# Kernel optimization log

Hardware: AMD Instinct MI355X
Metric: run time of the kernel (lower is better)

## Reference

```python
import jax, jax.numpy as jnp
import numpy as np

B, N, D = 2, 1024, 256
H, HD = 8, 32
FF = 1024
DEPTH = 2
RELH = 64  # rel-bias MLP hidden
SCALE = HD ** -0.5
EPS = 1e-5


def _ln(x, g, b):
    m = jnp.mean(x, axis=-1, keepdims=True)
    v = jnp.mean((x - m) ** 2, axis=-1, keepdims=True)
    return (x - m) * jax.lax.rsqrt(v + EPS) * g + b


def _rotary(n):
    half = HD // 2
    inv_freq = 1.0 / (10000.0 ** (jnp.arange(0, HD, 2, dtype=jnp.float32) / HD))  # [half]
    freqs = jnp.arange(n, dtype=jnp.float32)[:, None] * inv_freq[None, :]  # [n, half]
    return jnp.sin(freqs)[None, None], jnp.cos(freqs)[None, None]  # [1,1,n,half]


def _rope(t, sin, cos):
    t1, t2 = t[..., : HD // 2], t[..., HD // 2 :]
    return jnp.concatenate([t1 * cos - t2 * sin, t2 * cos + t1 * sin], axis=-1)


def setup_inputs() -> dict:
    key = jax.random.key(0)
    ks = jax.random.split(key, 20)
    s = 0.02
    inp = {
        "x": jax.random.normal(ks[0], (B, N, D), jnp.float32),
        "coords": jax.random.uniform(ks[1], (B, N, 2), jnp.float32),
        "velocities": jax.random.normal(ks[2], (B, N, 2), jnp.float32),
        "ln1_g": jnp.ones((DEPTH, D), jnp.float32),
        "ln1_b": jnp.zeros((DEPTH, D), jnp.float32),
        "Wqkv": jax.random.normal(ks[3], (DEPTH, D, 3 * H * HD), jnp.float32) * s,
        "relW1": jax.random.normal(ks[4], (DEPTH, 5, RELH), jnp.float32) * s,
        "relb1": jnp.zeros((DEPTH, RELH), jnp.float32),
        "relW2": jax.random.normal(ks[5], (DEPTH, RELH, H), jnp.float32) * s,
        "relb2": jnp.zeros((DEPTH, H), jnp.float32),
        "Wout": jax.random.normal(ks[6], (DEPTH, H * HD, D), jnp.float32) * s,
        "bout": jnp.zeros((DEPTH, D), jnp.float32),
        "ln2_g": jnp.ones((DEPTH, D), jnp.float32),
        "ln2_b": jnp.zeros((DEPTH, D), jnp.float32),
        "Wf1": jax.random.normal(ks[7], (DEPTH, D, FF), jnp.float32) * s,
        "bf1": jnp.zeros((DEPTH, FF), jnp.float32),
        "Wf2": jax.random.normal(ks[8], (DEPTH, FF, D), jnp.float32) * s,
        "bf2": jnp.zeros((DEPTH, D), jnp.float32),
    }
    return inp


def reference(x, coords, velocities, ln1_g, ln1_b, Wqkv, relW1, relb1, relW2,
              relb2, Wout, bout, ln2_g, ln2_b, Wf1, bf1, Wf2, bf2):
    sin, cos = _rotary(N)
    # pairwise relational features, shared across layers: [B,N,N,5]
    dx = coords[:, :, None, :] - coords[:, None, :, :]
    dist = jnp.linalg.norm(dx, axis=-1, keepdims=True)
    dv = velocities[:, :, None, :] - velocities[:, None, :, :]
    feats = jnp.concatenate([dx, dist, dv], axis=-1)
    for l in range(DEPTH):
        h = _ln(x, ln1_g[l], ln1_b[l])
        qkv = h @ Wqkv[l]  # [B,N,3*H*HD]
        q, k, v = jnp.split(qkv, 3, axis=-1)
        q, k, v = [t.reshape(B, N, H, HD).transpose(0, 2, 1, 3) for t in (q, k, v)]
        q = _rope(q, sin, cos)
        k = _rope(k, sin, cos)
        # relational bias MLP: [B,N,N,5] -> [B,N,N,H] -> [B,H,N,N]
        rel = jax.nn.gelu(feats @ relW1[l] + relb1[l], approximate=False) @ relW2[l] + relb2[l]
        rel = rel.transpose(0, 3, 1, 2)
        scores = jnp.einsum("bhid,bhjd->bhij", q, k) * SCALE + rel
        probs = jax.nn.softmax(scores, axis=-1)
        probs = jnp.nan_to_num(probs, nan=0.0)
        out = jnp.einsum("bhij,bhjd->bhid", probs, v)
        out = out.transpose(0, 2, 1, 3).reshape(B, N, H * HD)
        x = out @ Wout[l] + bout[l] + x
        h2 = _ln(x, ln2_g[l], ln2_b[l])
        x = jax.nn.gelu(h2 @ Wf1[l] + bf1[l], approximate=False) @ Wf2[l] + bf2[l] + x
    return x
```

## Files before the change

kernel.cpp:

```cpp
#include <hip/hip_runtime.h>
#include <math.h>

#define BN_ 2
#define NN 1024
#define DDIM 256
#define HH 8
#define HDIM 32
#define FFD 1024
#define EPSV 1e-5f
#define SCALEV 0.17677669529663687f

typedef __attribute__((ext_vector_type(8))) short s16x8;
typedef __attribute__((ext_vector_type(4))) short s16x4;
typedef __attribute__((ext_vector_type(4))) float f32x4;
typedef __attribute__((ext_vector_type(2))) _Float16 h2;
typedef __attribute__((ext_vector_type(8))) _Float16 f16x8;

__device__ __forceinline__ float gelu_f(float x){
  return 0.5f*x*(1.0f+erff(x*0.70710678118654752f));
}
__device__ __forceinline__ unsigned int pack_bf16(float lo, float hi){
  unsigned int ul = __float_as_uint(lo), uh = __float_as_uint(hi);
  ul += 0x7fff + ((ul>>16)&1);
  uh += 0x7fff + ((uh>>16)&1);
  return (ul>>16) | (uh & 0xffff0000u);
}
__device__ __forceinline__ unsigned short f2bf(float x){
  unsigned int u = __float_as_uint(x);
  u += 0x7fff + ((u>>16)&1);
  return (unsigned short)(u>>16);
}
__device__ __forceinline__ float bf2f(unsigned short u){
  return __uint_as_float(((unsigned int)u)<<16);
}
__device__ __forceinline__ unsigned int packtr(float lo, float hi){
  return __builtin_amdgcn_perm(__float_as_uint(hi), __float_as_uint(lo), 0x07060302u);
}
__device__ __forceinline__ f32x4 mfma16(s16x8 a, s16x8 b, f32x4 c){
  return __builtin_amdgcn_mfma_f32_16x16x32_bf16(a,b,c,0,0,0);
}
__device__ __forceinline__ f32x4 mfma16h(f16x8 a, f16x8 b, f32x4 c){
  return __builtin_amdgcn_mfma_f32_16x16x32_f16(a,b,c,0,0,0);
}

__global__ __launch_bounds__(256) void ln_kernel(const float* __restrict__ x,
    const float* __restrict__ g, const float* __restrict__ b,
    unsigned short* __restrict__ out){
  int row = blockIdx.x, tid = threadIdx.x;
  float val = x[(size_t)row*DDIM + tid];
  float s = val;
  #pragma unroll
  for (int o=32;o;o>>=1) s += __shfl_xor(s,o);
  __shared__ float sb[4], sb2[4];
  if ((tid&63)==0) sb[tid>>6]=s;
  __syncthreads();
  float mean = (sb[0]+sb[1]+sb[2]+sb[3]) * (1.0f/DDIM);
  float d = val-mean;
  float vs = d*d;
  #pragma unroll
  for (int o=32;o;o>>=1) vs += __shfl_xor(vs,o);
  if ((tid&63)==0) sb2[tid>>6]=vs;
  __syncthreads();
  float var = (sb2[0]+sb2[1]+sb2[2]+sb2[3]) * (1.0f/DDIM);
  out[(size_t)row*DDIM + tid] = f2bf(d*rsqrtf(var+EPSV)*g[tid]+b[tid]);
}

__global__ __launch_bounds__(256) void rope_table(float* __restrict__ sint, float* __restrict__ cost){
  int idx = blockIdx.x*256+threadIdx.x;
  int i = idx >> 4, d = idx & 15;
  float freq = (float)i * powf(10000.0f, -(float)d/16.0f);
  sint[idx]=sinf(freq); cost[idx]=cosf(freq);
}

__global__ __launch_bounds__(256) void wt_convert(const float* __restrict__ in,
    unsigned short* __restrict__ out, int K, int NC, int scaleCols, float scaleVal){
  __shared__ float tile[32][33];
  int tn0 = blockIdx.x*32;
  int tk0 = blockIdx.y*32;
  size_t loff = (size_t)blockIdx.z * K * NC;
  int t = threadIdx.x;
  int col = t & 31, rr = t >> 5;
  #pragma unroll
  for (int i=0;i<4;++i){
    int row = rr + i*8;
    tile[row][col] = in[loff + (size_t)(tk0+row)*NC + tn0+col];
  }
  __syncthreads();
  #pragma unroll
  for (int i=0;i<4;++i){
    int row = rr + i*8;
    int n = tn0 + row;
    float s = (n < scaleCols) ? scaleVal : 1.0f;
    out[loff + (size_t)n*K + tk0 + col] = f2bf(tile[col][row]*s);
  }
}

__global__ __launch_bounds__(256) void rope_apply_bf(const unsigned short* __restrict__ qkv,
    const float* __restrict__ sint, const float* __restrict__ cost,
    unsigned short* __restrict__ q, unsigned short* __restrict__ k,
    unsigned short* __restrict__ v){
  int row = blockIdx.x;
  int b = row>>10, i = row&1023;
  int tid = threadIdx.x; int h = tid>>5, d = tid&31;
  const unsigned short* base = qkv + (size_t)row*768;
  size_t oidx = (((size_t)((b<<3)+h)<<10) + i)*32 + d;
  v[oidx] = base[512 + h*32 + d];
  int dd = (d<16) ? d : d-16;
  float s = sint[i*16+dd], c = cost[i*16+dd];
  float q1 = bf2f(base[h*32+dd]), q2 = bf2f(base[h*32+dd+16]);
  q[oidx] = f2bf((d<16) ? (q1*c - q2*s) : (q2*c + q1*s));
  float k1 = bf2f(base[256+h*32+dd]), k2 = bf2f(base[256+h*32+dd+16]);
  k[oidx] = f2bf((d<16) ? (k1*c - k2*s) : (k2*c + k1*s));
}

__global__ __launch_bounds__(256) void rel_pre(const float* __restrict__ coords,
    const float* __restrict__ vel, const float* __restrict__ W1,
    const float* __restrict__ b1, const float* __restrict__ W2,
    _Float16* __restrict__ A, _Float16* __restrict__ A2,
    _Float16* __restrict__ W2T, _Float16* __restrict__ Wd){
  if (blockIdx.x == 512){
    int t = threadIdx.x;
    #pragma unroll
    for (int e=0;e<4;++e){
      int idx = t*4+e;
      int n = idx>>6, kk = idx&63;
      W2T[idx] = (n<8) ? (_Float16)W2[kk*8+n] : (_Float16)0.f;
    }
    if (t < 64) Wd[t] = (_Float16)W1[128+t];
    return;
  }
  int gid = blockIdx.x*256 + threadIdx.x;
  int node = gid >> 6, r = gid & 63;
  float c0 = coords[node*2], c1 = coords[node*2+1];
  float v0 = vel[node*2],    v1 = vel[node*2+1];
  float bv = c0*W1[r] + c1*W1[64+r] + v0*W1[192+r] + v1*W1[256+r];
  A[gid] = (_Float16)(b1[r] + bv);
  A2[gid] = (_Float16)bv;
}

__global__ __launch_bounds__(256, 4) void rel_fused7(const float* __restrict__ coords,
    const _Float16* __restrict__ A, const _Float16* __restrict__ A2,
    const _Float16* __restrict__ W2T, const _Float16* __restrict__ Wd,
    const float* __restrict__ b2, unsigned short* __restrict__ relbf){
  const int tid = threadIdx.x;
  const int bid = blockIdx.x;
  const int b = bid >> 9;
  const int ia = (bid & 511) * 2;
  const int w = tid>>6, l = tid&63, lc = l&15, lg = l>>4;
  const int nodea = (b<<10) + ia;
  float2 cia = *(const float2*)(coords + (size_t)nodea*2);
  float2 cib = *(const float2*)(coords + (size_t)nodea*2 + 2);

  union u4h { uint4 u; h2 h[4]; };
  u4h aA, aB, bA, bB, wA, wB;
  aA.u = *(const uint4*)(A + (size_t)nodea*64 + lg*8);
  aB.u = *(const uint4*)(A + (size_t)nodea*64 + 32 + lg*8);
  bA.u = *(const uint4*)(A + (size_t)(nodea+1)*64 + lg*8);
  bB.u = *(const uint4*)(A + (size_t)(nodea+1)*64 + 32 + lg*8);
  wA.u = *(const uint4*)(Wd + lg*8);
  wB.u = *(const uint4*)(Wd + 32 + lg*8);

  const f16x8 bf0 = *(const f16x8*)&W2T[lc*64 + lg*8];
  const f16x8 bf1 = *(const f16x8*)&W2T[lc*64 + 32 + lg*8];
  const float b2v = (lc<8) ? b2[lc] : 0.f;

  const h2 c2 = {(_Float16)0.0099735570f, (_Float16)0.0099735570f};
  const h2 c1 = {(_Float16)-0.0664904395f, (_Float16)-0.0664904395f};
  const h2 c0 = {(_Float16)0.3989422804f, (_Float16)0.3989422804f};
  const h2 ch = {(_Float16)0.5f, (_Float16)0.5f};

  const float* cb = coords + (size_t)((b<<10) + w*256 + lc)*2;
  const _Float16* ab = A2 + (size_t)((b<<10) + w*256 + lc)*64 + lg*8;
  unsigned short* oba = relbf + ((size_t)b<<23) + ((size_t)ia<<10)
                      + ((size_t)(lc&7)<<20) + (unsigned)(w*256 + lg*4);

  for (int st=0; st<16; ++st){
    u4h t0, t1;
    t0.u = *(const uint4*)(ab + st*1024);
    t1.u = *(const uint4*)(ab + st*1024 + 32);
    float2 cj = *(const float2*)(cb + st*32);
    {
      float dx = cia.x-cj.x, dy = cia.y-cj.y;
      _Float16 dh = (_Float16)sqrtf(fmaf(dx,dx,dy*dy));
      h2 d2 = {dh, dh};
      union { h2 h[4]; f16x8 v; } g0, g1;
      #pragma unroll
      for (int e=0;e<4;++e){
        h2 t = (aA.h[e] - t0.h[e]) + d2*wA.h[e];
        h2 u = t*t;
        h2 p = u*c2 + c1;
        p = u*p + c0;
        g0.h[e] = u*p + ch*t;
        h2 s = (aB.h[e] - t1.h[e]) + d2*wB.h[e];
        h2 v = s*s;
        h2 q = v*c2 + c1;
        q = v*q + c0;
        g1.h[e] = v*q + ch*s;
      }
      f32x4 z; z[0]=0.f; z[1]=0.f; z[2]=0.f; z[3]=0.f;
      z = mfma16h(g0.v, bf0, z);
      z = mfma16h(g1.v, bf1, z);
      if (lc < 8){
        unsigned short* op = oba + st*16;
        *(unsigned int*)op     = pack_bf16(z[0]+b2v, z[1]+b2v);
        *(unsigned int*)(op+2) = pack_bf16(z[2]+b2v, z[3]+b2v);
      }
    }
    {
      float dx = cib.x-cj.x, dy = cib.y-cj.y;
      _Float16 dh = (_Float16)sqrtf(fmaf(dx,dx,dy*dy));
      h2 d2 = {dh, dh};
      union { h2 h[4]; f16x8 v; } g0, g1;
      #pragma unroll
      for (int e=0;e<4;++e){
        h2 t = (bA.h[e] - t0.h[e]) + d2*wA.h[e];
        h2 u = t*t;
        h2 p = u*c2 + c1;
        p = u*p + c0;
        g0.h[e] = u*p + ch*t;
        h2 s = (bB.h[e] - t1.h[e]) + d2*wB.h[e];
        h2 v = s*s;
        h2 q = v*c2 + c1;
        q = v*q + c0;
        g1.h[e] = v*q + ch*s;
      }
      f32x4 z; z[0]=0.f; z[1]=0.f; z[2]=0.f; z[3]=0.f;
      z = mfma16h(g0.v, bf0, z);
      z = mfma16h(g1.v, bf1, z);
      if (lc < 8){
        unsigned short* op = oba + 1024 + st*16;
        *(unsigned int*)op     = pack_bf16(z[0]+b2v, z[1]+b2v);
        *(unsigned int*)(op+2) = pack_bf16(z[2]+b2v, z[3]+b2v);
      }
    }
  }
}

__global__ __launch_bounds__(256) void attn_mfma2(
    const unsigned short* __restrict__ q, const unsigned short* __restrict__ kk,
    const unsigned short* __restrict__ vv, const unsigned short* __restrict__ relbf,
    unsigned short* __restrict__ out){
  int bh = blockIdx.x >> 6;
  int i0 = (blockIdx.x & 63) * 16;
  int tid = threadIdx.x;
  int w = tid>>6, l = tid&63, lc = l&15, lg = l>>4;

  __shared__ __align__(16) float accL[4][2][16][17];
  __shared__ float mL[4][16];
  __shared__ float lL[4][16];

  const unsigned short* qb = q + ((size_t)(bh<<10) + i0)*32;
  const unsigned short* kb = kk + ((size_t)bh<<15);
  const unsigned short* vb = vv + ((size_t)bh<<15);
  const unsigned short* relrow = relbf + ((size_t)bh<<20) + ((size_t)(i0+lc)<<10);

  s16x8 qf = *(const s16x8*)(qb + (size_t)lc*32 + lg*8);

  float m = -1e30f, lsum = 0.f;
  f32x4 acc0, acc1;
  acc0[0]=0.f; acc0[1]=0.f; acc0[2]=0.f; acc0[3]=0.f;
  acc1 = acc0;

  for (int t=0; t<16; ++t){
    const int jt = w*256 + t*16;
    s16x8 kf = *(const s16x8*)(kb + (size_t)(jt+lc)*32 + lg*8);
    f32x4 z; z[0]=0.f; z[1]=0.f; z[2]=0.f; z[3]=0.f;
    f32x4 s = mfma16(kf, qf, z);
    ushort4 rl = *(const ushort4*)(relrow + jt + lg*4);
    s[0] += bf2f(rl.x); s[1] += bf2f(rl.y);
    s[2] += bf2f(rl.z); s[3] += bf2f(rl.w);
    float mx = fmaxf(fmaxf(s[0],s[1]), fmaxf(s[2],s[3]));
    mx = fmaxf(mx, __shfl_xor(mx,16));
    mx = fmaxf(mx, __shfl_xor(mx,32));
    float mn = fmaxf(m, mx);
    float scale = __expf(m - mn);
    m = mn;
    float p0 = __expf(s[0]-mn), p1 = __expf(s[1]-mn);
    float p2 = __expf(s[2]-mn), p3 = __expf(s[3]-mn);
    lsum = lsum*scale + (p0+p1+p2+p3);
    acc0[0]*=scale; acc0[1]*=scale; acc0[2]*=scale; acc0[3]*=scale;
    acc1[0]*=scale; acc1[1]*=scale; acc1[2]*=scale; acc1[3]*=scale;
#if __has_builtin(__builtin_amdgcn_mfma_f32_16x16x16bf16_1k)
    union { unsigned int u[2]; s16x4 v; } pu;
    pu.u[0] = packtr(p0,p1); pu.u[1] = packtr(p2,p3);
    const unsigned short* vp = vb + (size_t)(jt + lg*4)*32 + lc;
    s16x4 vf0, vf1;
    vf0[0]=(short)vp[0];  vf0[1]=(short)vp[32];  vf0[2]=(short)vp[64];  vf0[3]=(short)vp[96];
    vf1[0]=(short)vp[16]; vf1[1]=(short)vp[48];  vf1[2]=(short)vp[80];  vf1[3]=(short)vp[112];
    acc0 = __builtin_amdgcn_mfma_f32_16x16x16bf16_1k(vf0, pu.v, acc0, 0,0,0);
    acc1 = __builtin_amdgcn_mfma_f32_16x16x16bf16_1k(vf1, pu.v, acc1, 0,0,0);
#else
    unsigned int dw0 = packtr(p0,p1), dw1 = packtr(p2,p3);
    int src0 = lc + (((lg*2)&3)<<4);
    int src1 = lc + (((lg*2+1)&3)<<4);
    unsigned int u0 = __shfl(dw0, src0), u1 = __shfl(dw1, src0);
    unsigned int u2 = __shfl(dw0, src1), u3 = __shfl(dw1, src1);
    if (lg >= 2){ u0=0; u1=0; u2=0; u3=0; }
    union { unsigned int u[4]; s16x8 v; } pb;
    pb.u[0]=u0; pb.u[1]=u1; pb.u[2]=u2; pb.u[3]=u3;
    s16x8 vf0, vf1;
    #pragma unroll
    for (int e=0;e<8;++e){
      int j = (jt + lg*8 + e) & 1023;
      vf0[e] = (short)vb[(size_t)j*32 + lc];
      vf1[e] = (short)vb[(size_t)j*32 + 16 + lc];
    }
    acc0 = mfma16(vf0, pb.v, acc0);
    acc1 = mfma16(vf1, pb.v, acc1);
#endif
  }
  lsum += __shfl_xor(lsum, 16);
  lsum += __shfl_xor(lsum, 32);
  if (lg == 0){ mL[w][lc] = m; lL[w][lc] = lsum; }
  #pragma unroll
  for (int r=0;r<4;++r){
    accL[w][0][lg*4+r][lc] = acc0[r];
    accL[w][1][lg*4+r][lc] = acc1[r];
  }
  __syncthreads();
  int ii = tid & 15, dd = tid >> 4;
  float m0 = mL[0][ii], m1 = mL[1][ii], m2 = mL[2][ii], m3 = mL[3][ii];
  float ms = fmaxf(fmaxf(m0,m1), fmaxf(m2,m3));
  float e0 = __expf(m0-ms), e1 = __expf(m1-ms), e2 = __expf(m2-ms), e3 = __expf(m3-ms);
  float lt = lL[0][ii]*e0 + lL[1][ii]*e1 + lL[2][ii]*e2 + lL[3][ii]*e3;
  float a0 = accL[0][0][dd][ii]*e0 + accL[1][0][dd][ii]*e1
           + accL[2][0][dd][ii]*e2 + accL[3][0][dd][ii]*e3;
  float a1 = accL[0][1][dd][ii]*e0 + accL[1][1][dd][ii]*e1
           + accL[2][1][dd][ii]*e2 + accL[3][1][dd][ii]*e3;
  float inv = 1.0f/lt;
  int b = bh>>3, hh = bh&7;
  size_t ob2 = ((size_t)((b<<10)+i0+ii))*256 + hh*32;
  out[ob2 + dd]      = f2bf(a0*inv);
  out[ob2 + 16 + dd] = f2bf(a1*inv);
}

template<int K, int NC, int EPI, int BM, int BNt>
__global__ __launch_bounds__(256) void gemm_mfma(
    const unsigned short* __restrict__ Aa, const unsigned short* __restrict__ WT,
    const float* __restrict__ bias, const float* __restrict__ resid,
    void* __restrict__ outv){
  constexpr int WMm = BM/2, WNn = BNt/2;
  constexpr int FM = WMm/16, FN = WNn/16;
  constexpr int LP = 40;
  __shared__ __align__(16) unsigned short As[BM*LP];
  __shared__ __align__(16) unsigned short Bs[BNt*LP];
  const int tid = threadIdx.x;
  const int w = tid>>6, l = tid&63, lc = l&15, lg = l>>4;
  const int wm = w&1, wn = w>>1;
  const int n0 = blockIdx.x*BNt, m0 = blockIdx.y*BM;
  f32x4 acc[FM][FN];
  #pragma unroll
  for (int a=0;a<FM;++a)
    #pragma unroll
    for (int c=0;c<FN;++c){ acc[a][c][0]=0.f; acc[a][c][1]=0.f; acc[a][c][2]=0.f; acc[a][c][3]=0.f; }

  for (int k0=0; k0<K; k0+=32){
    __syncthreads();
    if constexpr (BM==64){
      int row = tid>>2, cg = tid&3;
      *(s16x8*)&As[row*LP+cg*8] = *(const s16x8*)&Aa[(size_t)(m0+row)*K + k0 + cg*8];
    } else {
      int row = tid>>3, cg = tid&7;
      *(ushort4*)&As[row*LP+cg*4] = *(const ushort4*)&Aa[(size_t)(m0+row)*K + k0 + cg*4];
    }
    if constexpr (BNt==64){
      int row = tid>>2, cg = tid&3;
      *(s16x8*)&Bs[row*LP+cg*8] = *(const s16x8*)&WT[(size_t)(n0+row)*K + k0 + cg*8];
    } else {
      int row = tid>>3, cg = tid&7;
      *(ushort4*)&Bs[row*LP+cg*4] = *(const ushort4*)&WT[(size_t)(n0+row)*K + k0 + cg*4];
    }
    __syncthreads();
    s16x8 af[FM], bv[FN];
    #pragma unroll
    for (int a=0;a<FM;++a) af[a] = *(const s16x8*)&As[(wm*WMm + a*16 + lc)*LP + lg*8];
    #pragma unroll
    for (int c=0;c<FN;++c) bv[c] = *(const s16x8*)&Bs[(wn*WNn + c*16 + lc)*LP + lg*8];
    #pragma unroll
    for (int a=0;a<FM;++a)
      #pragma unroll
      for (int c=0;c<FN;++c) acc[a][c] = mfma16(af[a], bv[c], acc[a][c]);
  }
  #pragma unroll
  for (int a=0;a<FM;++a){
    #pragma unroll
    for (int c=0;c<FN;++c){
      int n = n0 + wn*WNn + c*16 + lc;
      float bvv = (EPI!=0) ? bias[n] : 0.f;
      #pragma unroll
      for (int r=0;r<4;++r){
        int m = m0 + wm*WMm + a*16 + lg*4 + r;
        float vv = acc[a][c][r];
        if constexpr (EPI==0){
          ((unsigned short*)outv)[(size_t)m*NC + n] = f2bf(vv);
        } else if constexpr (EPI==1){
          ((float*)outv)[(size_t)m*NC + n] = vv + bvv + resid[(size_t)m*NC + n];
        } else {
          ((unsigned short*)outv)[(size_t)m*NC + n] = f2bf(gelu_f(vv + bvv));
        }
      }
    }
  }
}

extern "C" void kernel_launch(void* const* d_in, const int* in_sizes, int n_in,
                              void* d_out, int out_size, void* d_ws, size_t ws_size,
                              hipStream_t stream){
  const float* x_in  = (const float*)d_in[0];
  const float* coords= (const float*)d_in[1];
  const float* vel   = (const float*)d_in[2];
  const float* ln1_g = (const float*)d_in[3];
  const float* ln1_b = (const float*)d_in[4];
  const float* Wqkv  = (const float*)d_in[5];
  const float* relW1 = (const float*)d_in[6];
  const float* relb1 = (const float*)d_in[7];
  const float* relW2 = (const float*)d_in[8];
  const float* relb2 = (const float*)d_in[9];
  const float* Wout  = (const float*)d_in[10];
  const float* bout  = (const float*)d_in[11];
  const float* ln2_g = (const float*)d_in[12];
  const float* ln2_b = (const float*)d_in[13];
  const float* Wf1   = (const float*)d_in[14];
  const float* bf1   = (const float*)d_in[15];
  const float* Wf2   = (const float*)d_in[16];
  const float* bf2   = (const float*)d_in[17];

  float* x = (float*)d_out;
  unsigned short* us = (unsigned short*)d_ws;
  unsigned short* hbf   = us;
  unsigned short* qkvbf = hbf   + 524288;
  unsigned short* qbf   = qkvbf + 1572864;
  unsigned short* kbf   = qbf   + 524288;
  unsigned short* vbf   = kbf   + 524288;
  unsigned short* attbf = vbf   + 524288;
  unsigned short* midbf = attbf + 524288;
  unsigned short* relbf = midbf + 2097152;
  unsigned short* WqkvT = relbf + 16777216;
  unsigned short* WoutT = WqkvT + 393216;
  unsigned short* Wf1T  = WoutT + 131072;
  unsigned short* Wf2T  = Wf1T  + 524288;
  _Float16* W2Th = (_Float16*)(Wf2T + 524288);
  _Float16* Wdh  = W2Th + 1024;
  _Float16* Ah   = Wdh + 64;
  _Float16* A2h  = Ah + 131072;
  float* sint  = (float*)(A2h + 131072);
  float* cost  = sint + 16384;

  hipMemcpyAsync(x, x_in, sizeof(float)*524288, hipMemcpyDeviceToDevice, stream);
  rope_table<<<64,256,0,stream>>>(sint,cost);
  wt_convert<<<dim3(24,8,2),256,0,stream>>>(Wqkv, WqkvT, 256, 768, 256, SCALEV);
  wt_convert<<<dim3(8,8,2),256,0,stream>>>(Wout, WoutT, 256, 256, 0, 1.0f);
  wt_convert<<<dim3(32,8,2),256,0,stream>>>(Wf1, Wf1T, 256, 1024, 0, 1.0f);
  wt_convert<<<dim3(8,32,2),256,0,stream>>>(Wf2, Wf2T, 1024, 256, 0, 1.0f);

  for (int l=0;l<2;++l){
    ln_kernel<<<2048,256,0,stream>>>(x, ln1_g+l*256, ln1_b+l*256, hbf);
    gemm_mfma<256,768,0,64,64><<<dim3(12,32),256,0,stream>>>(
        hbf, WqkvT + (size_t)l*196608, nullptr, nullptr, qkvbf);
    rope_apply_bf<<<2048,256,0,stream>>>(qkvbf, sint, cost, qbf, kbf, vbf);
    rel_pre<<<513,256,0,stream>>>(coords, vel, relW1+l*320, relb1+l*64,
                                  relW2+l*512, Ah, A2h, W2Th, Wdh);
    rel_fused7<<<1024,256,0,stream>>>(coords, Ah, A2h, W2Th, Wdh,
                                      relb2+l*8, relbf);
    attn_mfma2<<<1024,256,0,stream>>>(qbf, kbf, vbf, relbf, attbf);
    gemm_mfma<256,256,1,32,32><<<dim3(8,64),256,0,stream>>>(
        attbf, WoutT + (size_t)l*65536, bout+l*256, x, x);
    ln_kernel<<<2048,256,0,stream>>>(x, ln2_g+l*256, ln2_b+l*256, hbf);
    gemm_mfma<256,1024,2,64,64><<<dim3(16,32),256,0,stream>>>(
        hbf, Wf1T + (size_t)l*262144, bf1+l*1024, nullptr, midbf);
    gemm_mfma<1024,256,1,32,32><<<dim3(8,64),256,0,stream>>>(
        midbf, Wf2T + (size_t)l*262144, bf2+l*256, x, x);
  }
}
```

Measured before the change: 206.3 us.

## Pre-transpose V for vectorized attention loads and process four query rows per rel block

Adds a v_transpose kernel that writes V as [bh][d][j] into the now-free qkv buffer, so the attention kernel loads its PV operand fragments with single vector loads instead of strided scalar gathers. Separately, the relational-bias kernel now handles four query rows per block instead of two, halving the grid and reusing the loaded key-side features and coordinates across more rows. The cost is an extra kernel launch with its memory traffic, plus higher register use in the rel kernel, which may reduce occupancy.

```diff
diff --git a/kernel.cpp b/kernel.cpp
--- a/kernel.cpp
+++ b/kernel.cpp
@@ -113,6 +113,29 @@
   k[oidx] = f2bf((d<16) ? (k1*c - k2*s) : (k2*c + k1*s));
 }
 
+__global__ __launch_bounds__(256) void v_transpose(const unsigned short* __restrict__ v,
+    unsigned short* __restrict__ vt){
+  __shared__ unsigned short t[64][34];
+  int bh = blockIdx.x >> 4;
+  int j0 = (blockIdx.x & 15) << 6;
+  int tid = threadIdx.x;
+  const unsigned short* vb = v + ((size_t)bh<<15) + (size_t)j0*32;
+  {
+    int j = tid >> 2, dg = (tid & 3) * 8;
+    s16x8 r = *(const s16x8*)(vb + (size_t)j*32 + dg);
+    #pragma unroll
+    for (int e=0;e<8;++e) t[j][dg+e] = (unsigned short)r[e];
+  }
+  __syncthreads();
+  {
+    int d = tid >> 3, jg = (tid & 7) * 8;
+    s16x8 r;
+    #pragma unroll
+    for (int e=0;e<8;++e) r[e] = (short)t[jg+e][d];
+    *(s16x8*)(vt + (((size_t)bh*32 + d)<<10) + j0 + jg) = r;
+  }
+}
+
 __global__ __launch_bounds__(256) void rel_pre(const float* __restrict__ coords,
     const float* __restrict__ vel, const float* __restrict__ W1,
     const float* __restrict__ b1, const float* __restrict__ W2,
@@ -138,25 +161,28 @@
   A2[gid] = (_Float16)bv;
 }
 
-__global__ __launch_bounds__(256, 4) void rel_fused7(const float* __restrict__ coords,
+__global__ __launch_bounds__(256, 4) void rel_fused8(const float* __restrict__ coords,
     const _Float16* __restrict__ A, const _Float16* __restrict__ A2,
     const _Float16* __restrict__ W2T, const _Float16* __restrict__ Wd,
     const float* __restrict__ b2, unsigned short* __restrict__ relbf){
   const int tid = threadIdx.x;
   const int bid = blockIdx.x;
-  const int b = bid >> 9;
-  const int ia = (bid & 511) * 2;
+  const int b = bid >> 8;
+  const int ia = (bid & 255) * 4;
   const int w = tid>>6, l = tid&63, lc = l&15, lg = l>>4;
   const int nodea = (b<<10) + ia;
-  float2 cia = *(const float2*)(coords + (size_t)nodea*2);
-  float2 cib = *(const float2*)(coords + (size_t)nodea*2 + 2);
+
+  float2 ci[4];
+  #pragma unroll
+  for (int r=0;r<4;++r) ci[r] = *(const float2*)(coords + (size_t)(nodea+r)*2);
 
   union u4h { uint4 u; h2 h[4]; };
-  u4h aA, aB, bA, bB, wA, wB;
-  aA.u = *(const uint4*)(A + (size_t)nodea*64 + lg*8);
-  aB.u = *(const uint4*)(A + (size_t)nodea*64 + 32 + lg*8);
-  bA.u = *(const uint4*)(A + (size_t)(nodea+1)*64 + lg*8);
-  bB.u = *(const uint4*)(A + (size_t)(nodea+1)*64 + 32 + lg*8);
+  u4h aA[4], aB[4], wA, wB;
+  #pragma unroll
+  for (int r=0;r<4;++r){
+    aA[r].u = *(const uint4*)(A + (size_t)(nodea+r)*64 + lg*8);
+    aB[r].u = *(const uint4*)(A + (size_t)(nodea+r)*64 + 32 + lg*8);
+  }
   wA.u = *(const uint4*)(Wd + lg*8);
   wB.u = *(const uint4*)(Wd + 32 + lg*8);
 
@@ -179,66 +205,40 @@
     t0.u = *(const uint4*)(ab + st*1024);
     t1.u = *(const uint4*)(ab + st*1024 + 32);
     float2 cj = *(const float2*)(cb + st*32);
-    {
-      float dx = cia.x-cj.x, dy = cia.y-cj.y;
+    #pragma unroll
+    for (int r=0;r<4;++r){
+      float dx = ci[r].x-cj.x, dy = ci[r].y-cj.y;
       _Float16 dh = (_Float16)sqrtf(fmaf(dx,dx,dy*dy));
       h2 d2 = {dh, dh};
       union { h2 h[4]; f16x8 v; } g0, g1;
       #pragma unroll
       for (int e=0;e<4;++e){
-        h2 t = (aA.h[e] - t0.h[e]) + d2*wA.h[e];
+        h2 t = (aA[r].h[e] - t0.h[e]) + d2*wA.h[e];
         h2 u = t*t;
         h2 p = u*c2 + c1;
         p = u*p + c0;
         g0.h[e] = u*p + ch*t;
-        h2 s = (aB.h[e] - t1.h[e]) + d2*wB.h[e];
-        h2 v = s*s;
-        h2 q = v*c2 + c1;
-        q = v*q + c0;
-        g1.h[e] = v*q + ch*s;
+        h2 s = (aB[r].h[e] - t1.h[e]) + d2*wB.h[e];
+        h2 v2 = s*s;
+        h2 q = v2*c2 + c1;
+        q = v2*q + c0;
+        g1.h[e] = v2*q + ch*s;
       }
       f32x4 z; z[0]=0.f; z[1]=0.f; z[2]=0.f; z[3]=0.f;
       z = mfma16h(g0.v, bf0, z);
       z = mfma16h(g1.v, bf1, z);
       if (lc < 8){
-        unsigned short* op = oba + st*16;
+        unsigned short* op = oba + (size_t)r*1024 + st*16;
         *(unsigned int*)op     = pack_bf16(z[0]+b2v, z[1]+b2v);
         *(unsigned int*)(op+2) = pack_bf16(z[2]+b2v, z[3]+b2v);
       }
     }
-    {
-      float dx = cib.x-cj.x, dy = cib.y-cj.y;
-      _Float16 dh = (_Float16)sqrtf(fmaf(dx,dx,dy*dy));
-      h2 d2 = {dh, dh};
-      union { h2 h[4]; f16x8 v; } g0, g1;
-      #pragma unroll
-      for (int e=0;e<4;++e){
-        h2 t = (bA.h[e] - t0.h[e]) + d2*wA.h[e];
-        h2 u = t*t;
-        h2 p = u*c2 + c1;
-        p = u*p + c0;
-        g0.h[e] = u*p + ch*t;
-        h2 s = (bB.h[e] - t1.h[e]) + d2*wB.h[e];
-        h2 v = s*s;
-        h2 q = v*c2 + c1;
-        q = v*q + c0;
-        g1.h[e] = v*q + ch*s;
-      }
-      f32x4 z; z[0]=0.f; z[1]=0.f; z[2]=0.f; z[3]=0.f;
-      z = mfma16h(g0.v, bf0, z);
-      z = mfma16h(g1.v, bf1, z);
-      if (lc < 8){
-        unsigned short* op = oba + 1024 + st*16;
-        *(unsigned int*)op     = pack_bf16(z[0]+b2v, z[1]+b2v);
-        *(unsigned int*)(op+2) = pack_bf16(z[2]+b2v, z[3]+b2v);
-      }
-    }
-  }
-}
-
-__global__ __launch_bounds__(256) void attn_mfma2(
+  }
+}
+
+__global__ __launch_bounds__(256) void attn_mfma3(
     const unsigned short* __restrict__ q, const unsigned short* __restrict__ kk,
-    const unsigned short* __restrict__ vv, const unsigned short* __restrict__ relbf,
+    const unsigned short* __restrict__ vt, const unsigned short* __restrict__ relbf,
     unsigned short* __restrict__ out){
   int bh = blockIdx.x >> 6;
   int i0 = (blockIdx.x & 63) * 16;
@@ -251,7 +251,7 @@
 
   const unsigned short* qb = q + ((size_t)(bh<<10) + i0)*32;
   const unsigned short* kb = kk + ((size_t)bh<<15);
-  const unsigned short* vb = vv + ((size_t)bh<<15);
+  const unsigned short* vtb = vt + ((size_t)bh<<15);
   const unsigned short* relrow = relbf + ((size_t)bh<<20) + ((size_t)(i0+lc)<<10);
 
   s16x8 qf = *(const s16x8*)(qb + (size_t)lc*32 + lg*8);
@@ -283,10 +283,8 @@
 #if __has_builtin(__builtin_amdgcn_mfma_f32_16x16x16bf16_1k)
     union { unsigned int u[2]; s16x4 v; } pu;
     pu.u[0] = packtr(p0,p1); pu.u[1] = packtr(p2,p3);
-    const unsigned short* vp = vb + (size_t)(jt + lg*4)*32 + lc;
-    s16x4 vf0, vf1;
-    vf0[0]=(short)vp[0];  vf0[1]=(short)vp[32];  vf0[2]=(short)vp[64];  vf0[3]=(short)vp[96];
-    vf1[0]=(short)vp[16]; vf1[1]=(short)vp[48];  vf1[2]=(short)vp[80];  vf1[3]=(short)vp[112];
+    s16x4 vf0 = *(const s16x4*)(vtb + (size_t)lc*1024 + jt + lg*4);
+    s16x4 vf1 = *(const s16x4*)(vtb + (size_t)(16+lc)*1024 + jt + lg*4);
     acc0 = __builtin_amdgcn_mfma_f32_16x16x16bf16_1k(vf0, pu.v, acc0, 0,0,0);
     acc1 = __builtin_amdgcn_mfma_f32_16x16x16bf16_1k(vf1, pu.v, acc1, 0,0,0);
 #else
@@ -298,13 +296,8 @@
     if (lg >= 2){ u0=0; u1=0; u2=0; u3=0; }
     union { unsigned int u[4]; s16x8 v; } pb;
     pb.u[0]=u0; pb.u[1]=u1; pb.u[2]=u2; pb.u[3]=u3;
-    s16x8 vf0, vf1;
-    #pragma unroll
-    for (int e=0;e<8;++e){
-      int j = (jt + lg*8 + e) & 1023;
-      vf0[e] = (short)vb[(size_t)j*32 + lc];
-      vf1[e] = (short)vb[(size_t)j*32 + 16 + lc];
-    }
+    s16x8 vf0 = *(const s16x8*)(vtb + (size_t)lc*1024 + jt + lg*8);
+    s16x8 vf1 = *(const s16x8*)(vtb + (size_t)(16+lc)*1024 + jt + lg*8);
     acc0 = mfma16(vf0, pb.v, acc0);
     acc1 = mfma16(vf1, pb.v, acc1);
 #endif
@@ -445,6 +438,7 @@
   _Float16* A2h  = Ah + 131072;
   float* sint  = (float*)(A2h + 131072);
   float* cost  = sint + 16384;
+  unsigned short* vtbuf = qkvbf;
 
   hipMemcpyAsync(x, x_in, sizeof(float)*524288, hipMemcpyDeviceToDevice, stream);
   rope_table<<<64,256,0,stream>>>(sint,cost);
@@ -458,11 +452,12 @@
     gemm_mfma<256,768,0,64,64><<<dim3(12,32),256,0,stream>>>(
         hbf, WqkvT + (size_t)l*196608, nullptr, nullptr, qkvbf);
     rope_apply_bf<<<2048,256,0,stream>>>(qkvbf, sint, cost, qbf, kbf, vbf);
+    v_transpose<<<256,256,0,stream>>>(vbf, vtbuf);
     rel_pre<<<513,256,0,stream>>>(coords, vel, relW1+l*320, relb1+l*64,
                                   relW2+l*512, Ah, A2h, W2Th, Wdh);
-    rel_fused7<<<1024,256,0,stream>>>(coords, Ah, A2h, W2Th, Wdh,
-                                      relb2+l*8, relbf);
-    attn_mfma2<<<1024,256,0,stream>>>(qbf, kbf, vbf, relbf, attbf);
+    rel_fused8<<<512,256,0,stream>>>(coords, Ah, A2h, W2Th, Wdh,
+                                     relb2+l*8, relbf);
+    attn_mfma3<<<1024,256,0,stream>>>(qbf, kbf, vtbuf, relbf, attbf);
     gemm_mfma<256,256,1,32,32><<<dim3(8,64),256,0,stream>>>(
         attbf, WoutT + (size_t)l*65536, bout+l*256, x, x);
     ln_kernel<<<2048,256,0,stream>>>(x, ln2_g+l*256, ln2_b+l*256, hbf);
```

Result: slower. 235.5 us (+14.2%).
